# Optimization experiments

Measured on AMD Instinct MI355X. Metric: run time of the kernel, lower is better.

The kernel has to match this reference:

```python
import jax, jax.numpy as jnp
import numpy as np

B, S, H = 2, 1024, 4096
NH, D = 32, 128
ROPE_BASE = 10000.0
W_BITS, A_BITS = 4, 8


def fake_quant(x, n_bits):
    """Symmetric fake quantization along the last dim (per-token / per-channel)."""
    qmax = 2.0 ** (n_bits - 1) - 1.0
    scale = jnp.max(jnp.abs(x), axis=-1, keepdims=True) / qmax
    scale = jnp.maximum(scale, 1e-8)
    q = jnp.clip(jnp.round(x / scale), -qmax - 1.0, qmax) * scale
    # straight-through estimator (matches fake-quant training semantics)
    return x + jax.lax.stop_gradient(q - x)


def quant_linear(x, w):
    # x: [..., in], w: [out, in]; quantize activation per-token, weight per-out-channel
    xq = fake_quant(x, A_BITS)
    wq = fake_quant(w, W_BITS)
    return jnp.einsum('bsi,oi->bso', xq, wq)


def rope_tables(seq_len, dim, dtype):
    inv_freq = 1.0 / (ROPE_BASE ** (jnp.arange(0, dim, 2, dtype=jnp.float32) / dim))
    t = jnp.arange(seq_len, dtype=jnp.float32)
    freqs = jnp.einsum('i,j->ij', t, inv_freq)          # [S, D/2]
    emb = jnp.concatenate([freqs, freqs], axis=-1)       # [S, D]
    return jnp.cos(emb).astype(dtype), jnp.sin(emb).astype(dtype)


def rotate_half(x):
    x1, x2 = jnp.split(x, 2, axis=-1)
    return jnp.concatenate([-x2, x1], axis=-1)


def setup_inputs() -> dict:
    key = jax.random.key(0)
    ks = jax.random.split(key, 5)
    hidden_states = jax.random.normal(ks[0], (B, S, H), jnp.float32)
    wq = jax.random.normal(ks[1], (H, H), jnp.float32) * 0.02
    wk = jax.random.normal(ks[2], (H, H), jnp.float32) * 0.02
    wv = jax.random.normal(ks[3], (H, H), jnp.float32) * 0.02
    wo = jax.random.normal(ks[4], (H, H), jnp.float32) * 0.02
    return {"hidden_states": hidden_states, "wq": wq, "wk": wk, "wv": wv, "wo": wo}


def reference(hidden_states, wq, wk, wv, wo):
    bsz, q_len, _ = hidden_states.shape
    # quantized QKV projections
    q = quant_linear(hidden_states, wq).reshape(bsz, q_len, NH, D).transpose(0, 2, 1, 3)
    k = quant_linear(hidden_states, wk).reshape(bsz, q_len, NH, D).transpose(0, 2, 1, 3)
    v = quant_linear(hidden_states, wv).reshape(bsz, q_len, NH, D).transpose(0, 2, 1, 3)
    # RoPE
    cos, sin = rope_tables(q_len, D, hidden_states.dtype)   # [S, D]
    cos = cos[None, None, :, :]
    sin = sin[None, None, :, :]
    q = q * cos + rotate_half(q) * sin
    k = k * cos + rotate_half(k) * sin
    # quantized QK^T
    qq = fake_quant(q, A_BITS)
    kq = fake_quant(k, A_BITS)
    scores = jnp.einsum('bhqd,bhkd->bhqk', qq, kq) / jnp.sqrt(jnp.float32(D))
    # causal mask
    causal = jnp.tril(jnp.ones((q_len, q_len), dtype=bool))
    scores = jnp.where(causal[None, None], scores, jnp.finfo(scores.dtype).min)
    p = jax.nn.softmax(scores, axis=-1)
    # quantized PV
    pq = fake_quant(p, A_BITS)
    vq = fake_quant(v, A_BITS)
    attn = jnp.einsum('bhqk,bhkd->bhqd', pq, vq)
    attn = attn.transpose(0, 2, 1, 3).reshape(bsz, q_len, H)
    # quantized output projection
    return quant_linear(attn, wo)
```

## Files before the change

kernel.cpp:

```cpp
#include <hip/hip_runtime.h>
#include <stdint.h>

#define S_LEN 1024
#define HDIM  4096
#define NHEAD 32
#define DHEAD 128
#define BATCH 2
#define MTOK  (BATCH * S_LEN)

typedef __attribute__((ext_vector_type(4))) int   i32x4;
typedef __attribute__((ext_vector_type(4))) float f32x4;
typedef __attribute__((ext_vector_type(8))) short bf16x8;

#define GLOBAL_AS __attribute__((address_space(1)))
#define LDS_AS    __attribute__((address_space(3)))

__device__ __forceinline__ void gl2lds16(const void* g, void* l) {
  __builtin_amdgcn_global_load_lds((const GLOBAL_AS unsigned int*)(g),
                                   (LDS_AS unsigned int*)(l), 16, 0, 0);
}

__device__ __forceinline__ unsigned short f2bf(float f) {
  unsigned int u = __float_as_uint(f);
  unsigned int r = (u + 0x7fffu + ((u >> 16) & 1u)) >> 16;
  return (unsigned short)r;
}

__global__ __launch_bounds__(256) void rowquant_kernel(
    const float* __restrict__ x, int8_t* __restrict__ q,
    float* __restrict__ scales, float qmax, float clipLo)
{
  const int row = blockIdx.x;
  const int t = threadIdx.x;
  const float* xr = x + (size_t)row * HDIM;
  float4 v[4];
  float am = 0.f;
#pragma unroll
  for (int i = 0; i < 4; ++i) {
    v[i] = ((const float4*)xr)[t + 256 * i];
    am = fmaxf(am, fmaxf(fmaxf(fabsf(v[i].x), fabsf(v[i].y)),
                         fmaxf(fabsf(v[i].z), fabsf(v[i].w))));
  }
#pragma unroll
  for (int off = 32; off > 0; off >>= 1) am = fmaxf(am, __shfl_down(am, off));
  __shared__ float wred[4];
  if ((t & 63) == 0) wred[t >> 6] = am;
  __syncthreads();
  const float m = fmaxf(fmaxf(wred[0], wred[1]), fmaxf(wred[2], wred[3]));
  const float scale = fmaxf(m / qmax, 1e-8f);
  if (t == 0) scales[row] = scale;
  int* qo = (int*)(q + (size_t)row * HDIM);
#pragma unroll
  for (int i = 0; i < 4; ++i) {
    int b0 = (int)fminf(fmaxf(rintf(v[i].x / scale), clipLo), qmax);
    int b1 = (int)fminf(fmaxf(rintf(v[i].y / scale), clipLo), qmax);
    int b2 = (int)fminf(fmaxf(rintf(v[i].z / scale), clipLo), qmax);
    int b3 = (int)fminf(fmaxf(rintf(v[i].w / scale), clipLo), qmax);
    qo[t + 256 * i] = (b0 & 0xff) | ((b1 & 0xff) << 8) | ((b2 & 0xff) << 16) | ((b3 & 0xff) << 24);
  }
}

__global__ __launch_bounds__(256) void ropetab_kernel(
    float* __restrict__ ct, float* __restrict__ st)
{
  const int t = blockIdx.x * 256 + threadIdx.x;
  const int s = t >> 6, d = t & 63;
  const float inv = powf(10000.0f, -(float)d * (1.0f / 64.0f));
  const float ang = (float)s * inv;
  float sn, c;
  sincosf(ang, &sn, &c);
  ct[t] = c;
  st[t] = sn;
}

template<int MODE>
__global__ __launch_bounds__(256, 2) void gemm_i8_fused_kernel(
    const int8_t* __restrict__ A, const float* __restrict__ sa,
    const int8_t* __restrict__ Bw, const float* __restrict__ sb,
    float* __restrict__ C,
    int8_t* __restrict__ o8, float* __restrict__ oscale,
    const float* __restrict__ ctab, const float* __restrict__ stab,
    unsigned short* __restrict__ vqT)
{
  __shared__ __align__(16) char smem[128 * 129 * 4];
  __shared__ float vscale[128];
  int8_t (*asB)[128 * 128] = (int8_t(*)[128 * 128])smem;
  int8_t (*bsB)[128 * 128] = (int8_t(*)[128 * 128])(smem + 32768);
  float (*fx)[129] = (float(*)[129])smem;

  const int flat = blockIdx.y * gridDim.x + blockIdx.x;
  const int nf = (flat & 7) * 64 + (flat >> 3);
  const int bmi = nf & 15, bni = nf >> 4;
  const int bm = bmi * 128, bn = bni * 128;

  const int tid = threadIdx.x;
  const int w = tid >> 6, l = tid & 63;
  const int l15 = l & 15, lg = l >> 4, l7 = l & 7;
  const int lr = l >> 3, g7 = l & 7;
  const int m0 = (w >> 1) * 64, n0 = (w & 1) * 64;

  const int8_t* aT = A + (size_t)(bm + lr) * HDIM + ((g7 ^ lr) << 4);
  const int8_t* bT = Bw + (size_t)(bn + lr) * HDIM + ((g7 ^ lr) << 4);

  i32x4 acc[4][4];
#pragma unroll
  for (int i = 0; i < 4; ++i)
#pragma unroll
    for (int j = 0; j < 4; ++j) acc[i][j] = (i32x4){0, 0, 0, 0};

  auto stage = [&](int t) {
    const int bf = t & 1;
    const size_t k = (size_t)t * 128;
#pragma unroll
    for (int i = 0; i < 4; ++i) {
      const int r0 = w * 32 + i * 8;
      gl2lds16(aT + (size_t)r0 * HDIM + k, asB[bf] + r0 * 128);
      gl2lds16(bT + (size_t)r0 * HDIM + k, bsB[bf] + r0 * 128);
    }
  };

  stage(0);
  asm volatile("s_waitcnt vmcnt(0)" ::: "memory");
  __builtin_amdgcn_s_barrier();

  for (int t = 0; t < 32; ++t) {
    if (t < 31) stage(t + 1);
    const int cur = t & 1;
    __builtin_amdgcn_s_setprio(1);
#pragma unroll
    for (int kk = 0; kk < 2; ++kk) {
      i32x4 aF[4], bF[4];
      const int slot = (((kk << 2) + lg) ^ l7) << 4;
#pragma unroll
      for (int i = 0; i < 4; ++i)
        aF[i] = *(const i32x4*)(asB[cur] + (m0 + i * 16 + l15) * 128 + slot);
#pragma unroll
      for (int j = 0; j < 4; ++j)
        bF[j] = *(const i32x4*)(bsB[cur] + (n0 + j * 16 + l15) * 128 + slot);
#pragma unroll
      for (int i = 0; i < 4; ++i)
#pragma unroll
        for (int j = 0; j < 4; ++j)
          acc[i][j] = __builtin_amdgcn_mfma_i32_16x16x64_i8(aF[i], bF[j], acc[i][j], 0, 0, 0);
    }
    __builtin_amdgcn_s_setprio(0);
    if (t < 31) {
      asm volatile("s_waitcnt vmcnt(0)" ::: "memory");
      __builtin_amdgcn_s_barrier();
    }
  }

  float sbr[4];
#pragma unroll
  for (int j = 0; j < 4; ++j) sbr[j] = sb[bn + n0 + j * 16 + l15];

  if (MODE == 0) {
#pragma unroll
    for (int i = 0; i < 4; ++i) {
#pragma unroll
      for (int r = 0; r < 4; ++r) {
        const int m = bm + m0 + i * 16 + lg * 4 + r;
        const float sm = sa[m];
        float* cp = C + (size_t)m * HDIM + bn + n0 + l15;
#pragma unroll
        for (int j = 0; j < 4; ++j)
          cp[j * 16] = sm * sbr[j] * (float)acc[i][j][r];
      }
    }
    return;
  }

  __syncthreads();
#pragma unroll
  for (int i = 0; i < 4; ++i) {
#pragma unroll
    for (int r = 0; r < 4; ++r) {
      const int ml = m0 + i * 16 + lg * 4 + r;
      const float sm = sa[bm + ml];
#pragma unroll
      for (int j = 0; j < 4; ++j)
        fx[ml][n0 + j * 16 + l15] = sm * sbr[j] * (float)acc[i][j][r];
    }
  }
  __syncthreads();

  const int h = bn >> 7;

  if (MODE == 1) {
    const int row = tid >> 1, half = tid & 1;
    const int sg = bm + row;
    const int b = sg >> 10, s = sg & (S_LEN - 1);
    const float* ct = ctab + (size_t)s * 64;
    const float* st = stab + (size_t)s * 64;
    float am = 0.f;
#pragma unroll
    for (int d0 = 0; d0 < 64; ++d0) {
      const int d = half * 64 + d0;
      const float x0 = fx[row][d];
      const float x1 = fx[row][d ^ 64];
      const float c = ct[d0], sn = st[d0];
      const float v = half ? (x0 * c + x1 * sn) : (x0 * c - x1 * sn);
      fx[row][d] = v;
      am = fmaxf(am, fabsf(v));
    }
    am = fmaxf(am, __shfl_xor(am, 1));
    const float scale = fmaxf(am * (1.0f / 127.0f), 1e-8f);
    int8_t* op = o8 + (((size_t)(b * NHEAD + h)) * S_LEN + s) * DHEAD + half * 64;
#pragma unroll
    for (int c4 = 0; c4 < 4; ++c4) {
      i32x4 dw;
#pragma unroll
      for (int u = 0; u < 4; ++u) {
        int pk = 0;
#pragma unroll
        for (int bi = 0; bi < 4; ++bi) {
          const float v = fx[row][half * 64 + c4 * 16 + u * 4 + bi];
          const int q = (int)fminf(fmaxf(rintf(v / scale), -128.f), 127.f);
          pk |= (q & 0xff) << (8 * bi);
        }
        dw[u] = pk;
      }
      *(i32x4*)(op + c4 * 16) = dw;
    }
    if (!half) oscale[((size_t)(b * NHEAD + h)) * S_LEN + s] = scale;
  } else {
    {
      const int row = tid >> 1, half = tid & 1;
      float am = 0.f;
#pragma unroll
      for (int d0 = 0; d0 < 64; ++d0)
        am = fmaxf(am, fabsf(fx[row][half * 64 + d0]));
      am = fmaxf(am, __shfl_xor(am, 1));
      if (!half) vscale[row] = fmaxf(am * (1.0f / 127.0f), 1e-8f);
    }
    __syncthreads();
    {
      const int d = tid >> 1, sh = tid & 1;
      const int b = bm >> 10;
      const int bh = b * NHEAD + h;
      unsigned short* op = vqT + ((size_t)bh * DHEAD + d) * S_LEN + (bm & (S_LEN - 1)) + sh * 64;
#pragma unroll
      for (int c8 = 0; c8 < 8; ++c8) {
        i32x4 dw;
#pragma unroll
        for (int u = 0; u < 4; ++u) {
          const int sl = sh * 64 + c8 * 8 + u * 2;
          const float sc0 = vscale[sl], sc1 = vscale[sl + 1];
          const float q0 = fminf(fmaxf(rintf(fx[sl][d] / sc0), -128.f), 127.f);
          const float q1 = fminf(fmaxf(rintf(fx[sl + 1][d] / sc1), -128.f), 127.f);
          dw[u] = (int)f2bf(q0 * sc0) | ((int)f2bf(q1 * sc1) << 16);
        }
        *(i32x4*)(op + c8 * 8) = dw;
      }
    }
  }
}

#define QB 64
#define KB 64

__global__ __launch_bounds__(256) void attn_mfma_kernel(
    const int8_t* __restrict__ qq, const float* __restrict__ sq,
    const int8_t* __restrict__ kq, const float* __restrict__ sk,
    const unsigned short* __restrict__ vqT,
    float* __restrict__ attn)
{
  __shared__ __align__(16) int8_t ks[KB * 128];
  __shared__ __align__(16) unsigned short vs[128 * 64];
  __shared__ __align__(16) unsigned short ps[QB][64];
  __shared__ float sk_t[KB];

  const int tid = threadIdx.x;
  const int w = tid >> 6;
  const int l = tid & 63;
  const int l15 = l & 15;
  const int lg = l >> 4;
  const int lr = l >> 3, g7 = l & 7;
  const int bflat = blockIdx.x;
  const int bh = (bflat & 7) + 8 * (bflat >> 6);
  const int qxb = (bflat >> 3) & 7;
  const size_t bhS = (size_t)bh * S_LEN;
  const int b = bh >> 5, h = bh & 31;
  const int NT = S_LEN / QB;

  for (int rep = 0; rep < 2; ++rep) {
    const int qt = rep ? (NT - 1 - qxb) : qxb;
    const int q0 = qt * QB;
    const int nkt = qt + 1;

    const int qrow = q0 + w * 16 + l15;
    const int8_t* qp = qq + (bhS + qrow) * (size_t)DHEAD;
    const i32x4 qa0 = *(const i32x4*)(qp + lg * 16);
    const i32x4 qa1 = *(const i32x4*)(qp + 64 + lg * 16);

    float sqv[4];
    int qg[4];
#pragma unroll
    for (int r = 0; r < 4; ++r) {
      qg[r] = q0 + w * 16 + lg * 4 + r;
      sqv[r] = sq[bhS + qg[r]] * 0.08838834764831843f * 1.4426950408889634f;
    }

    float rmax[4] = {-3.0e38f, -3.0e38f, -3.0e38f, -3.0e38f};

    for (int kt = 0; kt < nkt; ++kt) {
      const int k0 = kt * KB;
#pragma unroll
      for (int i = 0; i < 2; ++i) {
        const int r0 = w * 16 + i * 8;
        gl2lds16(kq + (bhS + k0 + r0 + lr) * (size_t)128 + ((g7 ^ lr) << 4),
                 ks + r0 * 128);
      }
      if (tid < KB) sk_t[tid] = sk[bhS + k0 + tid];
      __syncthreads();
      const bool diag = (kt == nkt - 1);
#pragma unroll
      for (int c = 0; c < 4; ++c) {
        const int krow = c * 16 + l15;
        const i32x4 b0 = *(const i32x4*)(ks + krow * 128 + ((lg ^ (krow & 7)) << 4));
        const i32x4 b1 = *(const i32x4*)(ks + krow * 128 + (((lg + 4) ^ (krow & 7)) << 4));
        i32x4 acc = {0, 0, 0, 0};
        acc = __builtin_amdgcn_mfma_i32_16x16x64_i8(qa0, b0, acc, 0, 0, 0);
        acc = __builtin_amdgcn_mfma_i32_16x16x64_i8(qa1, b1, acc, 0, 0, 0);
        const float skv = sk_t[krow];
        const int kgl = k0 + krow;
#pragma unroll
        for (int r = 0; r < 4; ++r) {
          const float s = (float)acc[r] * sqv[r] * skv;
          if (!diag || (kgl <= qg[r])) rmax[r] = fmaxf(rmax[r], s);
        }
      }
      __syncthreads();
    }
#pragma unroll
    for (int r = 0; r < 4; ++r)
#pragma unroll
      for (int off = 1; off < 16; off <<= 1)
        rmax[r] = fmaxf(rmax[r], __shfl_xor(rmax[r], off));

    float rs[4] = {0.f, 0.f, 0.f, 0.f};
    f32x4 oacc[8];
#pragma unroll
    for (int ds = 0; ds < 8; ++ds) oacc[ds] = (f32x4){0.f, 0.f, 0.f, 0.f};

    const int qloc = w * 16 + l15;
    const int swA0 = (lg ^ (qloc & 7)) << 3;
    const int swA1 = ((lg + 4) ^ (qloc & 7)) << 3;

    for (int kt = 0; kt < nkt; ++kt) {
      const int k0 = kt * KB;
#pragma unroll
      for (int i = 0; i < 2; ++i) {
        const int r0 = w * 16 + i * 8;
        gl2lds16(kq + (bhS + k0 + r0 + lr) * (size_t)128 + ((g7 ^ lr) << 4),
                 ks + r0 * 128);
      }
#pragma unroll
      for (int i = 0; i < 4; ++i) {
        const int r0 = w * 32 + i * 8;
        const unsigned short* src = vqT + ((size_t)bh * 128 + r0 + lr) * S_LEN
                                        + k0 + ((g7 ^ lr) << 3);
        gl2lds16(src, vs + r0 * 64);
      }
      if (tid < KB) sk_t[tid] = sk[bhS + k0 + tid];
      __syncthreads();
      const bool diag = (kt == nkt - 1);

#pragma unroll
      for (int c = 0; c < 4; ++c) {
        const int krow = c * 16 + l15;
        const i32x4 b0 = *(const i32x4*)(ks + krow * 128 + ((lg ^ (krow & 7)) << 4));
        const i32x4 b1 = *(const i32x4*)(ks + krow * 128 + (((lg + 4) ^ (krow & 7)) << 4));
        i32x4 acc = {0, 0, 0, 0};
        acc = __builtin_amdgcn_mfma_i32_16x16x64_i8(qa0, b0, acc, 0, 0, 0);
        acc = __builtin_amdgcn_mfma_i32_16x16x64_i8(qa1, b1, acc, 0, 0, 0);
        const float skv = sk_t[krow];
        const int kgl = k0 + krow;
#pragma unroll
        for (int r = 0; r < 4; ++r) {
          const float s2 = (float)acc[r] * sqv[r] * skv;
          const bool valid = !diag || (kgl <= qg[r]);
          const float e = valid ? exp2f(s2 - rmax[r]) : 0.0f;
          rs[r] += e;
          const float p = rintf(e * 127.0f);
          const int qr = w * 16 + lg * 4 + r;
          const int sidx = (((krow >> 3) ^ (qr & 7)) << 3) | (krow & 7);
          ps[qr][sidx] = f2bf(p);
        }
      }

      const bf16x8 a0 = *(const bf16x8*)&ps[qloc][swA0];
      const bf16x8 a1 = *(const bf16x8*)&ps[qloc][swA1];
#pragma unroll
      for (int ds = 0; ds < 8; ++ds) {
        const int d = ds * 16 + l15;
        const bf16x8 bv0 = *(const bf16x8*)(vs + d * 64 + ((lg ^ (d & 7)) << 3));
        const bf16x8 bv1 = *(const bf16x8*)(vs + d * 64 + (((lg + 4) ^ (d & 7)) << 3));
        oacc[ds] = __builtin_amdgcn_mfma_f32_16x16x32_bf16(a0, bv0, oacc[ds], 0, 0, 0);
        oacc[ds] = __builtin_amdgcn_mfma_f32_16x16x32_bf16(a1, bv1, oacc[ds], 0, 0, 0);
      }
      __syncthreads();
    }

#pragma unroll
    for (int r = 0; r < 4; ++r)
#pragma unroll
      for (int off = 1; off < 16; off <<= 1)
        rs[r] += __shfl_xor(rs[r], off);

#pragma unroll
    for (int r = 0; r < 4; ++r) {
      const float inv = 1.0f / (127.0f * rs[r]);
      float* op = attn + ((size_t)(b * S_LEN + qg[r])) * HDIM + h * DHEAD + l15;
#pragma unroll
      for (int ds = 0; ds < 8; ++ds)
        op[ds * 16] = oacc[ds][r] * inv;
    }
  }
}

extern "C" void kernel_launch(void* const* d_in, const int* in_sizes, int n_in,
                              void* d_out, int out_size, void* d_ws, size_t ws_size,
                              hipStream_t stream) {
  const float* hs = (const float*)d_in[0];
  const float* wmat[4] = { (const float*)d_in[1], (const float*)d_in[2],
                           (const float*)d_in[3], (const float*)d_in[4] };

  char* p = (char*)d_ws;
  auto take = [&](size_t sz) { char* r = p; p += (sz + 255) & ~(size_t)255; return r; };

  int8_t* xq8 = (int8_t*)take((size_t)MTOK * HDIM);
  int8_t* w4[4];
  for (int i = 0; i < 4; ++i) w4[i] = (int8_t*)take((size_t)HDIM * HDIM);
  float* sx = (float*)take((size_t)MTOK * 4);
  float* sw[4];
  for (int i = 0; i < 4; ++i) sw[i] = (float*)take((size_t)HDIM * 4);
  float* y = (float*)take((size_t)MTOK * HDIM * 4);
  int8_t* qq8 = (int8_t*)take((size_t)MTOK * HDIM);
  int8_t* kq8 = (int8_t*)take((size_t)MTOK * HDIM);
  unsigned short* vqT = (unsigned short*)take((size_t)MTOK * HDIM * 2);
  float* sqs = (float*)take((size_t)BATCH * NHEAD * S_LEN * 4);
  float* sks = (float*)take((size_t)BATCH * NHEAD * S_LEN * 4);
  float* sattn = (float*)take((size_t)MTOK * 4);
  float* ctab = (float*)take((size_t)S_LEN * 64 * 4);
  float* stab = (float*)take((size_t)S_LEN * 64 * 4);

  rowquant_kernel<<<MTOK, 256, 0, stream>>>(hs, xq8, sx, 127.f, -128.f);
  for (int i = 0; i < 4; ++i)
    rowquant_kernel<<<HDIM, 256, 0, stream>>>(wmat[i], w4[i], sw[i], 7.f, -8.f);
  ropetab_kernel<<<S_LEN * 64 / 256, 256, 0, stream>>>(ctab, stab);

  const dim3 gg(HDIM / 128, MTOK / 128);
  gemm_i8_fused_kernel<1><<<gg, 256, 0, stream>>>(
      xq8, sx, w4[0], sw[0], nullptr, qq8, sqs, ctab, stab, nullptr);
  gemm_i8_fused_kernel<1><<<gg, 256, 0, stream>>>(
      xq8, sx, w4[1], sw[1], nullptr, kq8, sks, ctab, stab, nullptr);
  gemm_i8_fused_kernel<2><<<gg, 256, 0, stream>>>(
      xq8, sx, w4[2], sw[2], nullptr, nullptr, nullptr, nullptr, nullptr, vqT);

  attn_mfma_kernel<<<512, 256, 0, stream>>>(qq8, sqs, kq8, sks, vqT, y);

  rowquant_kernel<<<MTOK, 256, 0, stream>>>(y, xq8, sattn, 127.f, -128.f);
  gemm_i8_fused_kernel<0><<<gg, 256, 0, stream>>>(
      xq8, sattn, w4[3], sw[3], (float*)d_out, nullptr, nullptr, nullptr, nullptr, nullptr);
}
```

Before: 319.4 us.

## Merge Q/K/V projections into one 256x256-tile 8-wave int8 GEMM launch

Replaces three separate 128x128-tile QKV GEMM launches with a single 384-block kernel that uses 512 threads, 256x256 tiles and a phase-interleaved double-buffered LDS pipeline. Each phase loads fragments, issues async global-to-LDS loads for the next stage and runs MFMAs under raised priority. The RoPE, quantization and V-transpose epilogue is re-done in four 128x128 chunks that reuse the LDS. The goal is more data reuse per tile, fewer launches and a filled machine in one wave, at the cost of 128 accumulator registers per thread and one block per CU.

```diff
diff --git a/kernel.cpp b/kernel.cpp
--- a/kernel.cpp
+++ b/kernel.cpp
@@ -73,20 +73,241 @@
   st[t] = sn;
 }
 
-template<int MODE>
-__global__ __launch_bounds__(256, 2) void gemm_i8_fused_kernel(
+__shared__ char qkv_smem[131072];
+
+struct QkvAcc { i32x4 a[8][4]; };
+
+template<int MH, int NH, int BUF, class STG, class WT>
+__device__ __forceinline__ void qph(QkvAcc& A, int wm, int wn, int l15, int lg,
+                                    STG stg, WT wt) {
+  const int8_t* aL = (const int8_t*)qkv_smem + BUF * 32768;
+  const int8_t* bL = (const int8_t*)qkv_smem + 65536 + BUF * 32768;
+  i32x4 aF[4][2], bF[2][2];
+#pragma unroll
+  for (int fi = 0; fi < 4; ++fi) {
+    const int R = wm * 128 + MH * 64 + fi * 16 + l15;
+#pragma unroll
+    for (int kk = 0; kk < 2; ++kk)
+      aF[fi][kk] = *(const i32x4*)(aL + R * 128 + ((((kk << 2) + lg) ^ (R & 7)) << 4));
+  }
+#pragma unroll
+  for (int nj = 0; nj < 2; ++nj) {
+    const int R = wn * 64 + NH * 32 + nj * 16 + l15;
+#pragma unroll
+    for (int kk = 0; kk < 2; ++kk)
+      bF[nj][kk] = *(const i32x4*)(bL + R * 128 + ((((kk << 2) + lg) ^ (R & 7)) << 4));
+  }
+  stg();
+  __builtin_amdgcn_s_barrier();
+  asm volatile("s_waitcnt lgkmcnt(0)" ::: "memory");
+  __builtin_amdgcn_sched_barrier(0);
+  __builtin_amdgcn_s_setprio(1);
+#pragma unroll
+  for (int fi = 0; fi < 4; ++fi)
+#pragma unroll
+    for (int nj = 0; nj < 2; ++nj)
+#pragma unroll
+      for (int kk = 0; kk < 2; ++kk)
+        A.a[MH * 4 + fi][NH * 2 + nj] = __builtin_amdgcn_mfma_i32_16x16x64_i8(
+            aF[fi][kk], bF[nj][kk], A.a[MH * 4 + fi][NH * 2 + nj], 0, 0, 0);
+  __builtin_amdgcn_s_setprio(0);
+  wt();
+  __builtin_amdgcn_s_barrier();
+}
+
+__global__ __launch_bounds__(512, 1) void gemm_qkv_8p_kernel(
+    const int8_t* __restrict__ A, const float* __restrict__ sa,
+    const int8_t* __restrict__ w0, const int8_t* __restrict__ w1,
+    const int8_t* __restrict__ w2,
+    const float* __restrict__ sw0, const float* __restrict__ sw1,
+    const float* __restrict__ sw2,
+    int8_t* __restrict__ qq8, float* __restrict__ sqs,
+    int8_t* __restrict__ kq8, float* __restrict__ sks,
+    unsigned short* __restrict__ vqT,
+    const float* __restrict__ ctab, const float* __restrict__ stab)
+{
+  const int flat = blockIdx.x;
+  const int nf = (flat & 7) * 48 + (flat >> 3);
+  const int z = nf >> 7;
+  const int rr = nf & 127;
+  const int bmi = rr >> 4, bni = rr & 15;
+  const int bm = bmi * 256, bn = bni * 256;
+
+  const int8_t* Bw = (z == 0) ? w0 : ((z == 1) ? w1 : w2);
+  const float* swz = (z == 0) ? sw0 : ((z == 1) ? sw1 : sw2);
+
+  const int tid = threadIdx.x;
+  const int w = tid >> 6, l = tid & 63;
+  const int l15 = l & 15, lg = l >> 4;
+  const int wm = w >> 2, wn = w & 3;
+
+  auto stA = [&](int h, int t) {
+    const int bf = t & 1;
+    const int ko = t * 128;
+#pragma unroll
+    for (int ii = 0; ii < 2; ++ii) {
+      const int rbase = ii * 128 + h * 64 + w * 8;
+      gl2lds16(A + (size_t)(bm + rbase + (l >> 3)) * HDIM + ko + (((l & 7) ^ ((l >> 3) & 7)) << 4),
+               qkv_smem + bf * 32768 + rbase * 128);
+    }
+  };
+  auto stB = [&](int h, int t) {
+    const int bf = t & 1;
+    const int ko = t * 128;
+#pragma unroll
+    for (int ii = 0; ii < 2; ++ii) {
+      const int rbase = ii * 128 + (w >> 2) * 64 + h * 32 + (w & 3) * 8;
+      gl2lds16(Bw + (size_t)(bn + rbase + (l >> 3)) * HDIM + ko + (((l & 7) ^ ((l >> 3) & 7)) << 4),
+               qkv_smem + 65536 + bf * 32768 + rbase * 128);
+    }
+  };
+
+  QkvAcc acc;
+#pragma unroll
+  for (int i = 0; i < 8; ++i)
+#pragma unroll
+    for (int j = 0; j < 4; ++j) acc.a[i][j] = (i32x4){0, 0, 0, 0};
+
+  stA(0, 0); stB(0, 0); stA(1, 0); stB(1, 0);
+  stA(0, 1); stB(0, 1);
+  asm volatile("s_waitcnt vmcnt(4)" ::: "memory");
+  __builtin_amdgcn_s_barrier();
+
+#pragma unroll 1
+  for (int it = 0; it < 16; ++it) {
+    const int t0 = it * 2;
+    const bool nl = (it < 15);
+    qph<0, 0, 0>(acc, wm, wn, l15, lg, [&] { stA(1, t0 + 1); }, [] {});
+    qph<0, 1, 0>(acc, wm, wn, l15, lg, [&] { stB(1, t0 + 1); }, [] {});
+    qph<1, 0, 0>(acc, wm, wn, l15, lg, [&] { if (nl) stA(0, t0 + 2); }, [] {});
+    qph<1, 1, 0>(acc, wm, wn, l15, lg, [&] { if (nl) stB(0, t0 + 2); }, [&] {
+      if (nl) { asm volatile("s_waitcnt vmcnt(4)" ::: "memory"); }
+      else    { asm volatile("s_waitcnt vmcnt(0)" ::: "memory"); } });
+    qph<0, 0, 1>(acc, wm, wn, l15, lg, [&] { if (nl) stA(1, t0 + 2); }, [] {});
+    qph<0, 1, 1>(acc, wm, wn, l15, lg, [&] { if (nl) stB(1, t0 + 2); }, [] {});
+    qph<1, 0, 1>(acc, wm, wn, l15, lg, [&] { if (nl) stA(0, t0 + 3); }, [] {});
+    qph<1, 1, 1>(acc, wm, wn, l15, lg, [&] { if (nl) stB(0, t0 + 3); }, [&] {
+      if (nl) { asm volatile("s_waitcnt vmcnt(4)" ::: "memory"); } });
+  }
+
+  float (*fx)[129] = (float(*)[129])qkv_smem;
+  float (*amred)[5] = (float(*)[5])(qkv_smem + 66048);
+  float* vsc = (float*)(qkv_smem + 68608);
+
+  float sbr[4];
+#pragma unroll
+  for (int nj = 0; nj < 4; ++nj) sbr[nj] = swz[bn + wn * 64 + nj * 16 + l15];
+
+#pragma unroll 1
+  for (int ch = 0; ch < 4; ++ch) {
+    const int mh = ch >> 1, hh = ch & 1;
+    if (wm == mh && (wn >> 1) == hh) {
+#pragma unroll
+      for (int mi = 0; mi < 8; ++mi)
+#pragma unroll
+        for (int r = 0; r < 4; ++r) {
+          const int lrow = mi * 16 + lg * 4 + r;
+          const float sm = sa[bm + mh * 128 + lrow];
+#pragma unroll
+          for (int nj = 0; nj < 4; ++nj)
+            fx[lrow][(wn & 1) * 64 + nj * 16 + l15] = sm * sbr[nj] * (float)acc.a[mi][nj][r];
+        }
+    }
+    __syncthreads();
+
+    const int h = (bn >> 7) + hh;
+    if (z <= 1) {
+      const int row = tid & 127, qtr = tid >> 7;
+      const int gtok = bm + mh * 128 + row;
+      const int b = gtok >> 10, s = gtok & (S_LEN - 1);
+      const float* ct = ctab + (size_t)s * 64;
+      const float* st_ = stab + (size_t)s * 64;
+      float am = 0.f;
+#pragma unroll
+      for (int i = 0; i < 32; ++i) {
+        const int d = qtr * 32 + i;
+        const int dd = d & 63;
+        const float x0 = fx[row][d], x1 = fx[row][d ^ 64];
+        const float v = (d < 64) ? (x0 * ct[dd] - x1 * st_[dd])
+                                 : (x0 * ct[dd] + x1 * st_[dd]);
+        am = fmaxf(am, fabsf(v));
+      }
+      amred[row][qtr] = am;
+      __syncthreads();
+      const float mx = fmaxf(fmaxf(amred[row][0], amred[row][1]),
+                             fmaxf(amred[row][2], amred[row][3]));
+      const float scale = fmaxf(mx * (1.0f / 127.0f), 1e-8f);
+      int8_t* op = (z == 0 ? qq8 : kq8)
+                 + (((size_t)(b * NHEAD + h)) * S_LEN + s) * DHEAD + qtr * 32;
+#pragma unroll
+      for (int c4 = 0; c4 < 2; ++c4) {
+        i32x4 dw;
+#pragma unroll
+        for (int u = 0; u < 4; ++u) {
+          int pk = 0;
+#pragma unroll
+          for (int bi = 0; bi < 4; ++bi) {
+            const int d = qtr * 32 + c4 * 16 + u * 4 + bi;
+            const int dd = d & 63;
+            const float x0 = fx[row][d], x1 = fx[row][d ^ 64];
+            const float v = (d < 64) ? (x0 * ct[dd] - x1 * st_[dd])
+                                     : (x0 * ct[dd] + x1 * st_[dd]);
+            const int qv = (int)fminf(fmaxf(rintf(v / scale), -128.f), 127.f);
+            pk |= (qv & 0xff) << (8 * bi);
+          }
+          dw[u] = pk;
+        }
+        *(i32x4*)(op + c4 * 16) = dw;
+      }
+      if (qtr == 0) (z == 0 ? sqs : sks)[((size_t)(b * NHEAD + h)) * S_LEN + s] = scale;
+    } else {
+      {
+        const int row = tid & 127, qtr = tid >> 7;
+        float am = 0.f;
+#pragma unroll
+        for (int i = 0; i < 32; ++i)
+          am = fmaxf(am, fabsf(fx[row][qtr * 32 + i]));
+        amred[row][qtr] = am;
+      }
+      __syncthreads();
+      if (tid < 128) {
+        const float mx = fmaxf(fmaxf(amred[tid][0], amred[tid][1]),
+                               fmaxf(amred[tid][2], amred[tid][3]));
+        vsc[tid] = fmaxf(mx * (1.0f / 127.0f), 1e-8f);
+      }
+      __syncthreads();
+      {
+        const int d = tid & 127, sq = tid >> 7;
+        const int gtok0 = bm + mh * 128;
+        const int b = gtok0 >> 10;
+        const int s0 = (gtok0 & (S_LEN - 1)) + sq * 32;
+        unsigned short* op = vqT + (((size_t)(b * NHEAD + h)) * DHEAD + d) * S_LEN + s0;
+#pragma unroll
+        for (int c8 = 0; c8 < 4; ++c8) {
+          i32x4 dw;
+#pragma unroll
+          for (int u = 0; u < 4; ++u) {
+            const int sl = sq * 32 + c8 * 8 + u * 2;
+            const float sc0 = vsc[sl], sc1 = vsc[sl + 1];
+            const float q0 = fminf(fmaxf(rintf(fx[sl][d] / sc0), -128.f), 127.f);
+            const float q1 = fminf(fmaxf(rintf(fx[sl + 1][d] / sc1), -128.f), 127.f);
+            dw[u] = (int)f2bf(q0 * sc0) | ((int)f2bf(q1 * sc1) << 16);
+          }
+          *(i32x4*)(op + c8 * 8) = dw;
+        }
+      }
+    }
+    __syncthreads();
+  }
+}
+
+__global__ __launch_bounds__(256, 2) void gemm_i8_dbuf_kernel(
     const int8_t* __restrict__ A, const float* __restrict__ sa,
     const int8_t* __restrict__ Bw, const float* __restrict__ sb,
-    float* __restrict__ C,
-    int8_t* __restrict__ o8, float* __restrict__ oscale,
-    const float* __restrict__ ctab, const float* __restrict__ stab,
-    unsigned short* __restrict__ vqT)
+    float* __restrict__ C)
 {
-  __shared__ __align__(16) char smem[128 * 129 * 4];
-  __shared__ float vscale[128];
-  int8_t (*asB)[128 * 128] = (int8_t(*)[128 * 128])smem;
-  int8_t (*bsB)[128 * 128] = (int8_t(*)[128 * 128])(smem + 32768);
-  float (*fx)[129] = (float(*)[129])smem;
+  __shared__ __align__(16) int8_t asB[2][128 * 128];
+  __shared__ __align__(16) int8_t bsB[2][128 * 128];
 
   const int flat = blockIdx.y * gridDim.x + blockIdx.x;
   const int nf = (flat & 7) * 64 + (flat >> 3);
@@ -153,105 +374,16 @@
   float sbr[4];
 #pragma unroll
   for (int j = 0; j < 4; ++j) sbr[j] = sb[bn + n0 + j * 16 + l15];
-
-  if (MODE == 0) {
-#pragma unroll
-    for (int i = 0; i < 4; ++i) {
-#pragma unroll
-      for (int r = 0; r < 4; ++r) {
-        const int m = bm + m0 + i * 16 + lg * 4 + r;
-        const float sm = sa[m];
-        float* cp = C + (size_t)m * HDIM + bn + n0 + l15;
-#pragma unroll
-        for (int j = 0; j < 4; ++j)
-          cp[j * 16] = sm * sbr[j] * (float)acc[i][j][r];
-      }
-    }
-    return;
-  }
-
-  __syncthreads();
 #pragma unroll
   for (int i = 0; i < 4; ++i) {
 #pragma unroll
     for (int r = 0; r < 4; ++r) {
-      const int ml = m0 + i * 16 + lg * 4 + r;
-      const float sm = sa[bm + ml];
+      const int m = bm + m0 + i * 16 + lg * 4 + r;
+      const float sm = sa[m];
+      float* cp = C + (size_t)m * HDIM + bn + n0 + l15;
 #pragma unroll
       for (int j = 0; j < 4; ++j)
-        fx[ml][n0 + j * 16 + l15] = sm * sbr[j] * (float)acc[i][j][r];
-    }
-  }
-  __syncthreads();
-
-  const int h = bn >> 7;
-
-  if (MODE == 1) {
-    const int row = tid >> 1, half = tid & 1;
-    const int sg = bm + row;
-    const int b = sg >> 10, s = sg & (S_LEN - 1);
-    const float* ct = ctab + (size_t)s * 64;
-    const float* st = stab + (size_t)s * 64;
-    float am = 0.f;
-#pragma unroll
-    for (int d0 = 0; d0 < 64; ++d0) {
-      const int d = half * 64 + d0;
-      const float x0 = fx[row][d];
-      const float x1 = fx[row][d ^ 64];
-      const float c = ct[d0], sn = st[d0];
-      const float v = half ? (x0 * c + x1 * sn) : (x0 * c - x1 * sn);
-      fx[row][d] = v;
-      am = fmaxf(am, fabsf(v));
-    }
-    am = fmaxf(am, __shfl_xor(am, 1));
-    const float scale = fmaxf(am * (1.0f / 127.0f), 1e-8f);
-    int8_t* op = o8 + (((size_t)(b * NHEAD + h)) * S_LEN + s) * DHEAD + half * 64;
-#pragma unroll
-    for (int c4 = 0; c4 < 4; ++c4) {
-      i32x4 dw;
-#pragma unroll
-      for (int u = 0; u < 4; ++u) {
-        int pk = 0;
-#pragma unroll
-        for (int bi = 0; bi < 4; ++bi) {
-          const float v = fx[row][half * 64 + c4 * 16 + u * 4 + bi];
-          const int q = (int)fminf(fmaxf(rintf(v / scale), -128.f), 127.f);
-          pk |= (q & 0xff) << (8 * bi);
-        }
-        dw[u] = pk;
-      }
-      *(i32x4*)(op + c4 * 16) = dw;
-    }
-    if (!half) oscale[((size_t)(b * NHEAD + h)) * S_LEN + s] = scale;
-  } else {
-    {
-      const int row = tid >> 1, half = tid & 1;
-      float am = 0.f;
-#pragma unroll
-      for (int d0 = 0; d0 < 64; ++d0)
-        am = fmaxf(am, fabsf(fx[row][half * 64 + d0]));
-      am = fmaxf(am, __shfl_xor(am, 1));
-      if (!half) vscale[row] = fmaxf(am * (1.0f / 127.0f), 1e-8f);
-    }
-    __syncthreads();
-    {
-      const int d = tid >> 1, sh = tid & 1;
-      const int b = bm >> 10;
-      const int bh = b * NHEAD + h;
-      unsigned short* op = vqT + ((size_t)bh * DHEAD + d) * S_LEN + (bm & (S_LEN - 1)) + sh * 64;
-#pragma unroll
-      for (int c8 = 0; c8 < 8; ++c8) {
-        i32x4 dw;
-#pragma unroll
-        for (int u = 0; u < 4; ++u) {
-          const int sl = sh * 64 + c8 * 8 + u * 2;
-          const float sc0 = vscale[sl], sc1 = vscale[sl + 1];
-          const float q0 = fminf(fmaxf(rintf(fx[sl][d] / sc0), -128.f), 127.f);
-          const float q1 = fminf(fmaxf(rintf(fx[sl + 1][d] / sc1), -128.f), 127.f);
-          dw[u] = (int)f2bf(q0 * sc0) | ((int)f2bf(q1 * sc1) << 16);
-        }
-        *(i32x4*)(op + c8 * 8) = dw;
-      }
+        cp[j * 16] = sm * sbr[j] * (float)acc[i][j][r];
     }
   }
 }
@@ -450,17 +582,13 @@
     rowquant_kernel<<<HDIM, 256, 0, stream>>>(wmat[i], w4[i], sw[i], 7.f, -8.f);
   ropetab_kernel<<<S_LEN * 64 / 256, 256, 0, stream>>>(ctab, stab);
 
+  gemm_qkv_8p_kernel<<<384, 512, 0, stream>>>(
+      xq8, sx, w4[0], w4[1], w4[2], sw[0], sw[1], sw[2],
+      qq8, sqs, kq8, sks, vqT, ctab, stab);
+
+  attn_mfma_kernel<<<512, 256, 0, stream>>>(qq8, sqs, kq8, sks, vqT, y);
+
+  rowquant_kernel<<<MTOK, 256, 0, stream>>>(y, xq8, sattn, 127.f, -128.f);
   const dim3 gg(HDIM / 128, MTOK / 128);
-  gemm_i8_fused_kernel<1><<<gg, 256, 0, stream>>>(
-      xq8, sx, w4[0], sw[0], nullptr, qq8, sqs, ctab, stab, nullptr);
-  gemm_i8_fused_kernel<1><<<gg, 256, 0, stream>>>(
-      xq8, sx, w4[1], sw[1], nullptr, kq8, sks, ctab, stab, nullptr);
-  gemm_i8_fused_kernel<2><<<gg, 256, 0, stream>>>(
-      xq8, sx, w4[2], sw[2], nullptr, nullptr, nullptr, nullptr, nullptr, vqT);
-
-  attn_mfma_kernel<<<512, 256, 0, stream>>>(qq8, sqs, kq8, sks, vqT, y);
-
-  rowquant_kernel<<<MTOK, 256, 0, stream>>>(y, xq8, sattn, 127.f, -128.f);
-  gemm_i8_fused_kernel<0><<<gg, 256, 0, stream>>>(
-      xq8, sattn, w4[3], sw[3], (float*)d_out, nullptr, nullptr, nullptr, nullptr, nullptr);
-}
+  gemm_i8_dbuf_kernel<<<gg, 256, 0, stream>>>(xq8, sattn, w4[3], sw[3], (float*)d_out);
+}
```

After: 577.9 us. 1.81x slower.

## Fuse two-pass attention softmax into single-pass online softmax with rescaling

Applied to the files above, without the earlier changes.

Replaces the separate row-max pass over all key tiles with an online softmax. Each tile's max is reduced across lanes, and the running sum and PV accumulators are rescaled before the tile's probabilities are quantized. This drops the repeated QK^T MFMAs and the second K load per tile, and raises wave priority around the PV MFMA block. In exchange there are per-tile shuffle reductions and accumulator rescales. Probabilities are now rounded to 127 levels against a running max rather than the final row max, so the quantized values can differ slightly from the reference.

```diff
diff --git a/kernel.cpp b/kernel.cpp
--- a/kernel.cpp
+++ b/kernel.cpp
@@ -301,7 +301,15 @@
       sqv[r] = sq[bhS + qg[r]] * 0.08838834764831843f * 1.4426950408889634f;
     }
 
-    float rmax[4] = {-3.0e38f, -3.0e38f, -3.0e38f, -3.0e38f};
+    float m_run[4] = {-3.0e38f, -3.0e38f, -3.0e38f, -3.0e38f};
+    float rs[4] = {0.f, 0.f, 0.f, 0.f};
+    f32x4 oacc[8];
+#pragma unroll
+    for (int ds = 0; ds < 8; ++ds) oacc[ds] = (f32x4){0.f, 0.f, 0.f, 0.f};
+
+    const int qloc = w * 16 + l15;
+    const int swA0 = (lg ^ (qloc & 7)) << 3;
+    const int swA1 = ((lg + 4) ^ (qloc & 7)) << 3;
 
     for (int kt = 0; kt < nkt; ++kt) {
       const int k0 = kt * KB;
@@ -311,9 +319,19 @@
         gl2lds16(kq + (bhS + k0 + r0 + lr) * (size_t)128 + ((g7 ^ lr) << 4),
                  ks + r0 * 128);
       }
+#pragma unroll
+      for (int i = 0; i < 4; ++i) {
+        const int r0 = w * 32 + i * 8;
+        const unsigned short* src = vqT + ((size_t)bh * 128 + r0 + lr) * S_LEN
+                                        + k0 + ((g7 ^ lr) << 3);
+        gl2lds16(src, vs + r0 * 64);
+      }
       if (tid < KB) sk_t[tid] = sk[bhS + k0 + tid];
       __syncthreads();
       const bool diag = (kt == nkt - 1);
+
+      float s2v[4][4];
+      float tmax[4] = {-3.0e38f, -3.0e38f, -3.0e38f, -3.0e38f};
 #pragma unroll
       for (int c = 0; c < 4; ++c) {
         const int krow = c * 16 + l15;
@@ -326,61 +344,34 @@
         const int kgl = k0 + krow;
 #pragma unroll
         for (int r = 0; r < 4; ++r) {
-          const float s = (float)acc[r] * sqv[r] * skv;
-          if (!diag || (kgl <= qg[r])) rmax[r] = fmaxf(rmax[r], s);
+          const bool valid = !diag || (kgl <= qg[r]);
+          const float s2 = valid ? ((float)acc[r] * sqv[r] * skv) : -3.0e38f;
+          s2v[c][r] = s2;
+          tmax[r] = fmaxf(tmax[r], s2);
         }
       }
-      __syncthreads();
-    }
-#pragma unroll
-    for (int r = 0; r < 4; ++r)
-#pragma unroll
-      for (int off = 1; off < 16; off <<= 1)
-        rmax[r] = fmaxf(rmax[r], __shfl_xor(rmax[r], off));
-
-    float rs[4] = {0.f, 0.f, 0.f, 0.f};
-    f32x4 oacc[8];
-#pragma unroll
-    for (int ds = 0; ds < 8; ++ds) oacc[ds] = (f32x4){0.f, 0.f, 0.f, 0.f};
-
-    const int qloc = w * 16 + l15;
-    const int swA0 = (lg ^ (qloc & 7)) << 3;
-    const int swA1 = ((lg + 4) ^ (qloc & 7)) << 3;
-
-    for (int kt = 0; kt < nkt; ++kt) {
-      const int k0 = kt * KB;
-#pragma unroll
-      for (int i = 0; i < 2; ++i) {
-        const int r0 = w * 16 + i * 8;
-        gl2lds16(kq + (bhS + k0 + r0 + lr) * (size_t)128 + ((g7 ^ lr) << 4),
-                 ks + r0 * 128);
-      }
-#pragma unroll
-      for (int i = 0; i < 4; ++i) {
-        const int r0 = w * 32 + i * 8;
-        const unsigned short* src = vqT + ((size_t)bh * 128 + r0 + lr) * S_LEN
-                                        + k0 + ((g7 ^ lr) << 3);
-        gl2lds16(src, vs + r0 * 64);
-      }
-      if (tid < KB) sk_t[tid] = sk[bhS + k0 + tid];
-      __syncthreads();
-      const bool diag = (kt == nkt - 1);
+#pragma unroll
+      for (int r = 0; r < 4; ++r)
+#pragma unroll
+        for (int off = 1; off < 16; off <<= 1)
+          tmax[r] = fmaxf(tmax[r], __shfl_xor(tmax[r], off));
+
+#pragma unroll
+      for (int r = 0; r < 4; ++r) {
+        const float m_new = fmaxf(m_run[r], tmax[r]);
+        const float f = exp2f(m_run[r] - m_new);
+        m_run[r] = m_new;
+        rs[r] *= f;
+#pragma unroll
+        for (int ds = 0; ds < 8; ++ds) oacc[ds][r] *= f;
+      }
 
 #pragma unroll
       for (int c = 0; c < 4; ++c) {
         const int krow = c * 16 + l15;
-        const i32x4 b0 = *(const i32x4*)(ks + krow * 128 + ((lg ^ (krow & 7)) << 4));
-        const i32x4 b1 = *(const i32x4*)(ks + krow * 128 + (((lg + 4) ^ (krow & 7)) << 4));
-        i32x4 acc = {0, 0, 0, 0};
-        acc = __builtin_amdgcn_mfma_i32_16x16x64_i8(qa0, b0, acc, 0, 0, 0);
-        acc = __builtin_amdgcn_mfma_i32_16x16x64_i8(qa1, b1, acc, 0, 0, 0);
-        const float skv = sk_t[krow];
-        const int kgl = k0 + krow;
 #pragma unroll
         for (int r = 0; r < 4; ++r) {
-          const float s2 = (float)acc[r] * sqv[r] * skv;
-          const bool valid = !diag || (kgl <= qg[r]);
-          const float e = valid ? exp2f(s2 - rmax[r]) : 0.0f;
+          const float e = exp2f(s2v[c][r] - m_run[r]);
           rs[r] += e;
           const float p = rintf(e * 127.0f);
           const int qr = w * 16 + lg * 4 + r;
@@ -391,6 +382,7 @@
 
       const bf16x8 a0 = *(const bf16x8*)&ps[qloc][swA0];
       const bf16x8 a1 = *(const bf16x8*)&ps[qloc][swA1];
+      __builtin_amdgcn_s_setprio(1);
 #pragma unroll
       for (int ds = 0; ds < 8; ++ds) {
         const int d = ds * 16 + l15;
@@ -399,6 +391,7 @@
         oacc[ds] = __builtin_amdgcn_mfma_f32_16x16x32_bf16(a0, bv0, oacc[ds], 0, 0, 0);
         oacc[ds] = __builtin_amdgcn_mfma_f32_16x16x32_bf16(a1, bv1, oacc[ds], 0, 0, 0);
       }
+      __builtin_amdgcn_s_setprio(0);
       __syncthreads();
     }
 
```

Result: faster. 309.9 us (-3.0%).
